# Optimization experiments

Hardware: AMD Instinct MI355X
Metric: run time of the kernel (lower is better)

## Reference

```python
import jax, jax.numpy as jnp
import numpy as np

ORDER = 63
CODEBOOK_SIZE = 256
MIN_DATA = 1
N_ITER = 5
EPS = 1e-05
PERTURB = 1e-05


def setup_inputs() -> dict:
    key = jax.random.key(0)
    x = jax.random.normal(key, (131072, ORDER + 1), dtype=jnp.float32)
    return {"x": x}


def _e_step(x, cb, T):
    # squared euclidean distances via gram trick: (T, curr)
    d2 = jnp.sum(x * x, 1)[:, None] - 2.0 * (x @ cb.T) + jnp.sum(cb * cb, 1)[None, :]
    idx = jnp.argmin(d2, axis=1)
    xq = cb[idx]
    dist = jnp.sum((x - xq) ** 2) / T
    return idx, dist


def _m_step(x, idx, curr, key):
    D = x.shape[1]
    ones = jnp.ones((x.shape[0],), x.dtype)
    n_data = jax.ops.segment_sum(ones, idx, num_segments=curr)        # histc
    mask = n_data >= MIN_DATA
    sums = jax.ops.segment_sum(x, idx, num_segments=curr)             # scatter_add
    cent = sums / jnp.maximum(n_data, 1.0)[:, None]
    m = jnp.argmax(n_data)
    r = jax.random.normal(key, (curr, D), x.dtype) * PERTURB
    nm = (~mask).astype(x.dtype)
    # empty clusters reseeded from the largest cluster, perturbed
    new = jnp.where(mask[:, None], cent, cent[m][None, :] - r)
    cnt = jnp.sum(nm)
    corr = jnp.sum(r * nm[:, None], axis=0) / jnp.maximum(cnt, 1.0)
    new = new.at[m].add(jnp.where(cnt > 0, corr, jnp.zeros_like(corr)))
    return new


def _lbg(x):
    T, D = x.shape
    K = CODEBOOK_SIZE
    codebook = jnp.full((K, D), 1e10, x.dtype).at[0].set(jnp.mean(x, axis=0))
    distance = jnp.asarray(jnp.inf, x.dtype)
    base = jax.random.key(42)
    curr = 1
    split = 0
    while curr * 2 <= K:  # static loop over log2(K) binary splits
        key_s = jax.random.fold_in(base, split)
        kr, kloop = jax.random.split(key_s)
        r = jax.random.normal(kr, (curr, D), x.dtype) * PERTURB
        codebook = codebook.at[curr:2 * curr].set(codebook[:curr] - r).at[:curr].add(r)
        curr *= 2
        prev = distance

        def body(carry, n, curr=curr):
            cb, prev_d, dist, done, key = carry
            idx, d_new = _e_step(x, cb, T)
            change = jnp.abs(prev_d - d_new)
            conv = (n > 0) & (change / (d_new + 1e-16) < EPS)
            key, sub = jax.random.split(key)
            cb_new = _m_step(x, idx, curr, sub)
            stop = done | conv
            cb_out = jnp.where(stop, cb, cb_new)        # skip m-step on convergence/break
            dist_out = jnp.where(done, dist, d_new)     # distance assigned before break
            prev_out = jnp.where(stop, prev_d, d_new)
            return (cb_out, prev_out, dist_out, stop, key), None

        carry0 = (codebook[:curr], prev, distance, jnp.asarray(False), kloop)
        (cb_fin, _, distance, _, _), _ = jax.lax.scan(body, carry0, jnp.arange(N_ITER))
        codebook = codebook.at[:curr].set(cb_fin)
        split += 1
    return codebook, distance


def reference(x):
    return _lbg(x)
```

## Files before the change

### kernel.cpp

```cpp
#include <hip/hip_runtime.h>
#include <stdint.h>


#define NPTS 131072
#define DIMS 64
#define KCB  256
#define NCB  16

struct LbgState { float dist; float prev; unsigned int done; unsigned int k0, k1; unsigned int pad; };

__device__ __forceinline__ uint32_t rotl32(uint32_t v, int n){ return (v<<n)|(v>>(32-n)); }

__device__ __forceinline__ void tf2x32(uint32_t k0, uint32_t k1, uint32_t x0, uint32_t x1,
                                       uint32_t& o0, uint32_t& o1){
  uint32_t ks2 = k0 ^ k1 ^ 0x1BD11BDAu;
  x0 += k0; x1 += k1;
  #define TFR(r) { x0 += x1; x1 = rotl32(x1, r); x1 ^= x0; }
  TFR(13) TFR(15) TFR(26) TFR(6)
  x0 += k1; x1 += ks2 + 1u;
  TFR(17) TFR(29) TFR(16) TFR(24)
  x0 += ks2; x1 += k0 + 2u;
  TFR(13) TFR(15) TFR(26) TFR(6)
  x0 += k0; x1 += k1 + 3u;
  TFR(17) TFR(29) TFR(16) TFR(24)
  x0 += k1; x1 += ks2 + 4u;
  TFR(13) TFR(15) TFR(26) TFR(6)
  x0 += ks2; x1 += k0 + 5u;
  #undef TFR
  o0 = x0; o1 = x1;
}

__device__ __forceinline__ float xla_erfinv_f32(float x){
  float w = -log1pf(-x*x);
  float p;
  if (w < 5.0f){
    w = w - 2.5f;
    p = 2.81022636e-08f;
    p = fmaf(p, w, 3.43273939e-07f);
    p = fmaf(p, w, -3.5233877e-06f);
    p = fmaf(p, w, -4.39150654e-06f);
    p = fmaf(p, w, 0.00021858087f);
    p = fmaf(p, w, -0.00125372503f);
    p = fmaf(p, w, -0.00417768164f);
    p = fmaf(p, w, 0.246640727f);
    p = fmaf(p, w, 1.50140941f);
  } else {
    w = sqrtf(w) - 3.0f;
    p = -0.000200214257f;
    p = fmaf(p, w, 0.000100950558f);
    p = fmaf(p, w, 0.00134934322f);
    p = fmaf(p, w, -0.00367342844f);
    p = fmaf(p, w, 0.00573950773f);
    p = fmaf(p, w, -0.0076224613f);
    p = fmaf(p, w, 0.00943887047f);
    p = fmaf(p, w, 1.00167406f);
    p = fmaf(p, w, 2.83297682f);
  }
  return p * x;
}

__device__ __forceinline__ float jax_normal_elem(uint32_t k0, uint32_t k1, uint32_t j){
  uint32_t o0, o1; tf2x32(k0, k1, 0u, j, o0, o1);
  uint32_t bits = o0 ^ o1;
  uint32_t fb = (bits >> 9) | 0x3f800000u;
  float f = __uint_as_float(fb) - 1.0f;
  const float lo = -0.99999994f;
  float u = f * 2.0f + lo;
  u = fmaxf(lo, u);
  return 1.41421356f * xla_erfinv_f32(u);
}

__device__ void do_split(float* __restrict__ cb, float* __restrict__ cnorm,
                         unsigned long long* __restrict__ sums,
                         unsigned int* __restrict__ ndata,
                         unsigned long long* __restrict__ distacc,
                         LbgState* __restrict__ st, int curr, int split, int t){
  __shared__ uint32_t kr0s, kr1s;
  if (t == 0){
    uint32_t ks0, ks1, a0, a1, b0, b1;
    tf2x32(0u, 42u, 0u, (uint32_t)split, ks0, ks1);
    tf2x32(ks0, ks1, 0u, 0u, a0, a1);
    tf2x32(ks0, ks1, 0u, 1u, b0, b1);
    kr0s = a0; kr1s = a1;
    st->k0 = b0; st->k1 = b1;
    st->prev = st->dist;
    st->done = 0u;
  }
  __syncthreads();
  const int n = curr * DIMS;
  for (int e = t; e < n; e += 256){
    int c = e >> 6, d = e & 63;
    float rv = jax_normal_elem(kr0s, kr1s, (uint32_t)e) * 1e-5f;
    float old = cb[c*DIMS + d];
    cb[(curr + c)*DIMS + d] = old - rv;
    cb[c*DIMS + d]          = old + rv;
  }
  __syncthreads();
  const int c2 = curr * 2;
  for (int c = t; c < c2; c += 256){
    float s = 0.f;
    for (int d = 0; d < DIMS; d++){ float vv = cb[c*DIMS+d]; s += vv*vv; }
    cnorm[c] = s;
  }
  for (int e = t; e < c2*DIMS; e += 256) sums[e] = 0ull;
  for (int c = t; c < c2; c += 256) ndata[c] = 0u;
  if (t == 0) *distacc = 0ull;
}

__global__ void mean_kernel(const float* __restrict__ x, unsigned long long* __restrict__ macc,
                            float* __restrict__ cb, float* __restrict__ cnorm,
                            unsigned long long* __restrict__ sums,
                            unsigned int* __restrict__ ndata,
                            unsigned long long* __restrict__ distacc,
                            LbgState* __restrict__ st, unsigned int* __restrict__ mcnt){
  __shared__ double part[256];
  __shared__ float stage[16*64];
  __shared__ int islast;
  const int t = threadIdx.x;
  const int d = t & 63;
  const int w = t >> 6;
  const size_t base = (size_t)blockIdx.x * 1024;
  const int lrow = t >> 4;
  const int lcol = (t & 15) * 4;

  const float4* xg = reinterpret_cast<const float4*>(x);
  float4 nxt = xg[((base + lrow) * DIMS + lcol) >> 2];
  double s = 0.0;
  for (int tt = 0; tt < 64; tt++){
    float4 cur = nxt;
    if (tt < 63)
      nxt = xg[((base + (tt+1)*16 + lrow) * DIMS + lcol) >> 2];
    __syncthreads();
    *reinterpret_cast<float4*>(&stage[lrow*DIMS + lcol]) = cur;
    __syncthreads();
    s += (double)stage[(w    )*DIMS + d];
    s += (double)stage[(w + 4)*DIMS + d];
    s += (double)stage[(w + 8)*DIMS + d];
    s += (double)stage[(w +12)*DIMS + d];
  }
  part[t] = s;
  __syncthreads();
  if (t < 64){
    double tot = part[t] + part[64+t] + part[128+t] + part[192+t];
    atomicAdd(&macc[t], (unsigned long long)__double2ll_rn(tot * 1099511627776.0));
  }
  __threadfence();
  __syncthreads();
  if (t == 0) islast = (atomicAdd(mcnt, 1u) == (unsigned)(gridDim.x - 1));
  __syncthreads();
  if (!islast) return;

  if (t < 64){
    long long mv = (long long)atomicAdd(&macc[t], 0ull);
    double mean = (double)mv * (1.0/1099511627776.0) / 131072.0;
    cb[t] = (float)mean;
  }
  for (int e = t; e < KCB*DIMS; e += 256)
    if (e >= 64) cb[e] = 1e10f;
  if (t == 0){
    st->dist = __builtin_inff();
    st->prev = __builtin_inff();
    st->done = 0u;
    atomicExch(mcnt, 0u);
  }
  __syncthreads();
  do_split(cb, cnorm, sums, ndata, distacc, st, 1, 0, t);
}

template<int CURR>
__global__ __launch_bounds__(256, 4)
void estep_kernel(const float* __restrict__ x, const float* __restrict__ cb,
                  const float* __restrict__ cnorm, unsigned char* __restrict__ bidx8,
                  unsigned long long* __restrict__ distacc, const LbgState* __restrict__ st){
  if (st->done) return;
  const int t = threadIdx.x;
  const int lane = t & 63;
  const int p = blockIdx.x * 256 + t;

  float xv[DIMS];
  const float4* xp = reinterpret_cast<const float4*>(x + (size_t)p * DIMS);
  #pragma unroll
  for (int i = 0; i < 16; i++){
    float4 v = xp[i];
    xv[4*i+0] = v.x; xv[4*i+1] = v.y; xv[4*i+2] = v.z; xv[4*i+3] = v.w;
  }
  float xx = 0.f;
  #pragma unroll
  for (int d = 0; d < DIMS; d++) xx += xv[d] * xv[d];

  constexpr int NJ = (CURR < 4) ? CURR : 4;
  float best = __builtin_inff();
  int bi = 0;
  for (int j0 = 0; j0 < CURR; j0 += NJ){
    const float* crow = cb + (size_t)j0 * DIMS;
    float acc[NJ];
    #pragma unroll
    for (int k = 0; k < NJ; k++) acc[k] = 0.f;
    #pragma unroll
    for (int d = 0; d < DIMS; d++){
      #pragma unroll
      for (int k = 0; k < NJ; k++)
        acc[k] = fmaf(xv[d], crow[k*DIMS + d], acc[k]);
    }
    #pragma unroll
    for (int k = 0; k < NJ; k++){
      float d2 = (xx - 2.0f*acc[k]) + cnorm[j0 + k];
      if (d2 < best){ best = d2; bi = j0 + k; }
    }
  }
  bidx8[p] = (unsigned char)bi;

  double dd = 0.0;
  const float4* cbv = reinterpret_cast<const float4*>(cb + (size_t)bi * DIMS);
  #pragma unroll
  for (int i = 0; i < 16; i++){
    float4 b = cbv[i];
    float df, sq;
    df = xv[4*i+0] - b.x; sq = df*df; dd += (double)sq;
    df = xv[4*i+1] - b.y; sq = df*df; dd += (double)sq;
    df = xv[4*i+2] - b.z; sq = df*df; dd += (double)sq;
    df = xv[4*i+3] - b.w; sq = df*df; dd += (double)sq;
  }
  for (int off = 32; off > 0; off >>= 1) dd += __shfl_down(dd, off);
  if (lane == 0)
    atomicAdd(distacc, (unsigned long long)__double2ll_rn(dd * 4294967296.0));
}

template<int CURR>
__global__ __launch_bounds__(256, 4)
void estep_sw(const float* __restrict__ x, const float* __restrict__ cb,
              const float* __restrict__ cnorm, unsigned char* __restrict__ bidx8,
              unsigned long long* __restrict__ distacc, const LbgState* __restrict__ st){
  if (st->done) return;
  constexpr int CPW = CURR / 4;
  constexpr int NJG = (CPW < 16) ? CPW : 16;
  constexpr int NG = CPW / NJG;
  __shared__ float4 xs[16*128];
  __shared__ float sxx[128];
  __shared__ float sbest[4*128];
  __shared__ int   sidx [4*128];
  __shared__ unsigned char sbidx[128];
  const int t = threadIdx.x;
  const int lane = t & 63;
  const int w = __builtin_amdgcn_readfirstlane(t >> 6);
  const int pbase = blockIdx.x * 128;

  {
    const int p = t & 127, h = t >> 7;
    const float4* xg = reinterpret_cast<const float4*>(x) + (size_t)(pbase + p) * 16 + h * 8;
    #pragma unroll
    for (int j = 0; j < 8; j++)
      xs[(h*8 + j)*128 + p] = xg[j];
  }
  __syncthreads();
  if (t < 128){
    float xx = 0.f;
    #pragma unroll
    for (int k4 = 0; k4 < 16; k4++){
      float4 v = xs[k4*128 + t];
      xx = fmaf(v.x, v.x, xx); xx = fmaf(v.y, v.y, xx);
      xx = fmaf(v.z, v.z, xx); xx = fmaf(v.w, v.w, xx);
    }
    sxx[t] = xx;
  }
  __syncthreads();

  const float xx0 = sxx[lane];
  const float xx1 = sxx[64 + lane];
  float best0 = __builtin_inff(), best1 = __builtin_inff();
  int bi0 = 0, bi1 = 0;
  const float4* cbg = reinterpret_cast<const float4*>(cb);
  const int cwbase = w * CPW;

  for (int g = 0; g < NG; g++){
    const int c0 = cwbase + g*NJG;
    float acc0[NJG], acc1[NJG];
    #pragma unroll
    for (int cj = 0; cj < NJG; cj++){ acc0[cj] = 0.f; acc1[cj] = 0.f; }
    for (int k4 = 0; k4 < 16; k4++){
      float4 xf0 = xs[k4*128 + lane];
      float4 xf1 = xs[k4*128 + 64 + lane];
      #pragma unroll
      for (int cj = 0; cj < NJG; cj++){
        float4 cf = cbg[(size_t)(c0 + cj)*16 + k4];
        acc0[cj] = fmaf(xf0.x, cf.x, acc0[cj]);
        acc0[cj] = fmaf(xf0.y, cf.y, acc0[cj]);
        acc0[cj] = fmaf(xf0.z, cf.z, acc0[cj]);
        acc0[cj] = fmaf(xf0.w, cf.w, acc0[cj]);
        acc1[cj] = fmaf(xf1.x, cf.x, acc1[cj]);
        acc1[cj] = fmaf(xf1.y, cf.y, acc1[cj]);
        acc1[cj] = fmaf(xf1.z, cf.z, acc1[cj]);
        acc1[cj] = fmaf(xf1.w, cf.w, acc1[cj]);
      }
    }
    #pragma unroll
    for (int cj = 0; cj < NJG; cj++){
      float cn = cnorm[c0 + cj];
      float d20 = (xx0 - 2.0f*acc0[cj]) + cn;
      if (d20 < best0){ best0 = d20; bi0 = c0 + cj; }
      float d21 = (xx1 - 2.0f*acc1[cj]) + cn;
      if (d21 < best1){ best1 = d21; bi1 = c0 + cj; }
    }
  }
  sbest[w*128 + lane]      = best0;  sidx[w*128 + lane]      = bi0;
  sbest[w*128 + 64 + lane] = best1;  sidx[w*128 + 64 + lane] = bi1;
  __syncthreads();

  if (t < 128){
    float best = sbest[t];
    int bi = sidx[t];
    #pragma unroll
    for (int ww = 1; ww < 4; ww++){
      float ob = sbest[ww*128 + t];
      int   oi = sidx [ww*128 + t];
      if (ob < best){ best = ob; bi = oi; }
    }
    sbidx[t] = (unsigned char)bi;
    bidx8[pbase + t] = (unsigned char)bi;
    const float4* cbv = cbg + (size_t)bi * 16;
    double dd = 0.0;
    #pragma unroll
    for (int k4 = 0; k4 < 16; k4++){
      float4 xv = xs[k4*128 + t];
      float4 b = cbv[k4];
      float df, sq;
      df = xv.x - b.x; sq = df*df; dd += (double)sq;
      df = xv.y - b.y; sq = df*df; dd += (double)sq;
      df = xv.z - b.z; sq = df*df; dd += (double)sq;
      df = xv.w - b.w; sq = df*df; dd += (double)sq;
    }
    for (int off = 32; off > 0; off >>= 1) dd += __shfl_down(dd, off);
    if ((t & 63) == 0)
      atomicAdd(distacc, (unsigned long long)__double2ll_rn(dd * 4294967296.0));
  }
}

template<int CURR, int NBLK>
__global__ __launch_bounds__(256)
void gather_kernel(const float* __restrict__ x, const unsigned char* __restrict__ bidx8,
                   unsigned long long* __restrict__ sums, unsigned int* __restrict__ ndata,
                   const LbgState* __restrict__ st){
  if (st->done) return;
  constexpr int CLOG = __builtin_ctz(CURR);
  constexpr int NCHUNK = NBLK / CURR;
  constexpr int PPC = NPTS / NCHUNK;
  constexpr int NPW = PPC / 4;
  __shared__ long long sacc[4][64][4];
  __shared__ unsigned int scw[4];
  const int t = threadIdx.x;
  const int lane = t & 63;
  const int w = t >> 6;
  const int c = blockIdx.x & (CURR - 1);
  const int chunk = blockIdx.x >> CLOG;
  const int pbase = chunk * PPC + w * NPW;
  const int sub = lane >> 4;
  const int dof = (lane & 15) * 4;

  long long a0 = 0, a1 = 0, a2 = 0, a3 = 0;
  unsigned int cnt = 0;
  int q0=0,q1=0,q2=0,q3=0,q4=0,q5=0,q6=0,q7=0, qn=0;
  const uint32_t* bp = reinterpret_cast<const uint32_t*>(bidx8 + pbase);
  for (int i = 0; i < NPW; i += 256){
    const uint32_t b4 = bp[(i >> 2) + lane];
    #pragma unroll
    for (int s = 0; s < 4; s++){
      unsigned long long m = __ballot(((b4 >> (8*s)) & 255u) == (unsigned)c);
      cnt += (unsigned int)__popcll(m);
      while (m){
        const int bit = __builtin_ctzll(m);
        m &= m - 1ull;
        const int p = pbase + i + bit*4 + s;
        if      (qn == 0) q0 = p;
        else if (qn == 1) q1 = p;
        else if (qn == 2) q2 = p;
        else if (qn == 3) q3 = p;
        else if (qn == 4) q4 = p;
        else if (qn == 5) q5 = p;
        else if (qn == 6) q6 = p;
        else              q7 = p;
        qn++;
        if (qn == 8){
          const int rA = (sub==0)?q0:(sub==1)?q1:(sub==2)?q2:q3;
          const int rB = (sub==0)?q4:(sub==1)?q5:(sub==2)?q6:q7;
          const float4 vA = *reinterpret_cast<const float4*>(x + (size_t)rA * DIMS + dof);
          const float4 vB = *reinterpret_cast<const float4*>(x + (size_t)rB * DIMS + dof);
          a0 += (long long)__double2int_rn((double)vA.x * 1048576.0);
          a1 += (long long)__double2int_rn((double)vA.y * 1048576.0);
          a2 += (long long)__double2int_rn((double)vA.z * 1048576.0);
          a3 += (long long)__double2int_rn((double)vA.w * 1048576.0);
          a0 += (long long)__double2int_rn((double)vB.x * 1048576.0);
          a1 += (long long)__double2int_rn((double)vB.y * 1048576.0);
          a2 += (long long)__double2int_rn((double)vB.z * 1048576.0);
          a3 += (long long)__double2int_rn((double)vB.w * 1048576.0);
          qn = 0;
        }
      }
    }
  }
  if (qn > 0){
    const int i1 = (qn > 1) ? q1 : q0;
    const int i2 = (qn > 2) ? q2 : q0;
    const int i3 = (qn > 3) ? q3 : q0;
    const int i4 = (qn > 4) ? q4 : q0;
    const int i5 = (qn > 5) ? q5 : q0;
    const int i6 = (qn > 6) ? q6 : q0;
    const int rA = (sub==0)?q0:(sub==1)?i1:(sub==2)?i2:i3;
    const int rB = (sub==0)?i4:(sub==1)?i5:(sub==2)?i6:q0;
    const float4 vA = *reinterpret_cast<const float4*>(x + (size_t)rA * DIMS + dof);
    const float4 vB = *reinterpret_cast<const float4*>(x + (size_t)rB * DIMS + dof);
    if (sub < qn){
      a0 += (long long)__double2int_rn((double)vA.x * 1048576.0);
      a1 += (long long)__double2int_rn((double)vA.y * 1048576.0);
      a2 += (long long)__double2int_rn((double)vA.z * 1048576.0);
      a3 += (long long)__double2int_rn((double)vA.w * 1048576.0);
    }
    if (sub + 4 < qn){
      a0 += (long long)__double2int_rn((double)vB.x * 1048576.0);
      a1 += (long long)__double2int_rn((double)vB.y * 1048576.0);
      a2 += (long long)__double2int_rn((double)vB.z * 1048576.0);
      a3 += (long long)__double2int_rn((double)vB.w * 1048576.0);
    }
  }
  sacc[w][lane][0] = a0; sacc[w][lane][1] = a1;
  sacc[w][lane][2] = a2; sacc[w][lane][3] = a3;
  if (lane == 0) scw[w] = cnt;
  __syncthreads();
  if (w == 0){
    long long tot = 0;
    #pragma unroll
    for (int ww = 0; ww < 4; ww++)
      #pragma unroll
      for (int r = 0; r < 4; r++)
        tot += sacc[ww][r*16 + (lane >> 2)][lane & 3];
    if (tot) atomicAdd(&sums[c*DIMS + lane], (unsigned long long)(tot * 1048576ll));
    if (lane == 0){
      unsigned int ct = scw[0] + scw[1] + scw[2] + scw[3];
      if (ct) atomicAdd(&ndata[c], ct);
    }
  }
}

__global__ void control_kernel(float* __restrict__ cb, float* __restrict__ cnorm,
                               const unsigned long long* __restrict__ sums_in,
                               unsigned long long* __restrict__ sums_out,
                               const unsigned int* __restrict__ ndata_in,
                               unsigned int* __restrict__ ndata_out,
                               const unsigned long long* __restrict__ distacc_in,
                               unsigned long long* __restrict__ distacc_out,
                               const LbgState* __restrict__ st_in,
                               LbgState* __restrict__ st_out,
                               int curr, int n_iter, int next_split){
  __shared__ float cm[64];
  __shared__ int redv[256];
  __shared__ int redi[256];
  __shared__ int s_m, s_cnt;
  const int t = threadIdx.x;
  const int b = blockIdx.x;

  const unsigned int done0 = st_in->done;
  float d_new = 0.f;
  int stop = 1;
  uint32_t sub0 = 0, sub1 = 0, nk0 = 0, nk1 = 0;
  if (!done0){
    double ddv = (double)(long long)(*distacc_in) * (1.0/4294967296.0);
    float sf = (float)ddv;
    d_new = sf / 131072.0f;
    float change = fabsf(st_in->prev - d_new);
    int conv = (n_iter > 0) && (change / (d_new + 1e-16f) < 1e-5f);
    stop = conv;
    if (!conv){
      tf2x32(st_in->k0, st_in->k1, 0u, 0u, nk0, nk1);
      tf2x32(st_in->k0, st_in->k1, 0u, 1u, sub0, sub1);
    }
  }

  const int rpb = (curr + NCB - 1) / NCB;
  const int r0 = b * rpb;
  int r1 = r0 + rpb; if (r1 > curr) r1 = curr;

  if (!done0 && !stop){
    int v = (t < curr) ? (int)ndata_in[t] : -1;
    redv[t] = v; redi[t] = t;
    __syncthreads();
    for (int s = 128; s > 0; s >>= 1){
      if (t < s){
        if (redv[t+s] > redv[t] || (redv[t+s] == redv[t] && redi[t+s] < redi[t])){
          redv[t] = redv[t+s]; redi[t] = redi[t+s];
        }
      }
      __syncthreads();
    }
    if (t == 0) s_m = redi[0];
    __syncthreads();
    redv[t] = (t < curr && ndata_in[t] == 0u) ? 1 : 0;
    __syncthreads();
    for (int s = 128; s > 0; s >>= 1){
      if (t < s) redv[t] += redv[t+s];
      __syncthreads();
    }
    if (t == 0) s_cnt = redv[0];
    __syncthreads();
    const int m = s_m;
    const int cntE = s_cnt;

    if (t < 64){
      unsigned int nm_ = ndata_in[m]; if (nm_ < 1u) nm_ = 1u;
      double cd = (double)(long long)sums_in[m*DIMS + t] * (1.0/1099511627776.0) / (double)nm_;
      cm[t] = (float)cd;
    }
    __syncthreads();

    for (int e = r0*DIMS + t; e < r1*DIMS; e += 256){
      int cc = e >> 6, d = e & 63;
      if (cc == m) continue;
      float nv;
      unsigned int nd = ndata_in[cc];
      if (nd >= 1u){
        double cd = (double)(long long)sums_in[e] * (1.0/1099511627776.0) / (double)nd;
        nv = (float)cd;
      } else {
        float rv = jax_normal_elem(sub0, sub1, (uint32_t)e) * 1e-5f;
        nv = cm[d] - rv;
      }
      cb[e] = nv;
    }
    if (m >= r0 && m < r1 && t < 64){
      float add = 0.f;
      if (cntE > 0){
        float acc = 0.f;
        for (int cc = 0; cc < curr; cc++){
          if (ndata_in[cc] == 0u)
            acc += jax_normal_elem(sub0, sub1, (uint32_t)(cc*DIMS + t)) * 1e-5f;
        }
        add = acc / fmaxf((float)cntE, 1.0f);
      }
      cb[m*DIMS + t] = cm[t] + add;
    }
    __syncthreads();

    for (int cc = r0 + t; cc < r1; cc += 256){
      float s = 0.f;
      for (int d = 0; d < DIMS; d++){ float vv = cb[cc*DIMS+d]; s += vv*vv; }
      cnorm[cc] = s;
    }
  }

  const int rows_next = (n_iter == 4 && curr < KCB) ? 2*curr : curr;
  for (int e = b*256 + t; e < rows_next*DIMS; e += NCB*256) sums_out[e] = 0ull;
  for (int cc = b*256 + t; cc < rows_next; cc += NCB*256) ndata_out[cc] = 0u;
  if (b == 0 && t == 0) *distacc_out = 0ull;

  if (b == 0 && t == 0){
    const float fin_dist = done0 ? st_in->dist : d_new;
    LbgState ns;
    ns.dist = fin_dist;
    if (done0 || stop){
      ns.prev = st_in->prev; ns.done = 1u; ns.k0 = st_in->k0; ns.k1 = st_in->k1;
    } else {
      ns.prev = d_new; ns.done = 0u; ns.k0 = nk0; ns.k1 = nk1;
    }
    ns.pad = 0u;
    if (n_iter == 4){
      if (curr < KCB){
        uint32_t ks0, ks1, sa0, sa1, sb0, sb1;
        tf2x32(0u, 42u, 0u, (uint32_t)next_split, ks0, ks1);
        tf2x32(ks0, ks1, 0u, 0u, sa0, sa1);
        tf2x32(ks0, ks1, 0u, 1u, sb0, sb1);
        ns.k0 = sb0; ns.k1 = sb1;
        ns.prev = fin_dist;
        ns.done = 0u;
      } else {
        cb[KCB*DIMS] = fin_dist;
      }
    }
    *st_out = ns;
  }

  if (n_iter == 4 && curr < KCB){
    uint32_t ks0, ks1, kr0, kr1, t0, t1;
    tf2x32(0u, 42u, 0u, (uint32_t)next_split, ks0, ks1);
    tf2x32(ks0, ks1, 0u, 0u, kr0, kr1);
    (void)t0; (void)t1;
    __syncthreads();
    for (int e = r0*DIMS + t; e < r1*DIMS; e += 256){
      int cc = e >> 6, d = e & 63;
      float rv = jax_normal_elem(kr0, kr1, (uint32_t)e) * 1e-5f;
      float old = cb[e];
      cb[(curr + cc)*DIMS + d] = old - rv;
      cb[e]                    = old + rv;
    }
    __syncthreads();
    for (int cc = r0 + t; cc < r1; cc += 256){
      float s0 = 0.f, s1 = 0.f;
      for (int d = 0; d < DIMS; d++){
        float v0 = cb[cc*DIMS + d];        s0 += v0*v0;
        float v1 = cb[(curr+cc)*DIMS + d]; s1 += v1*v1;
      }
      cnorm[cc] = s0;
      cnorm[curr + cc] = s1;
    }
  }
}

extern "C" void kernel_launch(void* const* d_in, const int* in_sizes, int n_in,
                              void* d_out, int out_size, void* d_ws, size_t ws_size,
                              hipStream_t stream){
  const float* x = (const float*)d_in[0];
  float* cb = (float*)d_out;
  char* ws = (char*)d_ws;
  unsigned long long* sums0   = (unsigned long long*)(ws + 0);
  unsigned long long* sums1   = (unsigned long long*)(ws + 131072);
  unsigned long long* macc    = (unsigned long long*)(ws + 262144);
  unsigned long long* dist0   = (unsigned long long*)(ws + 262656);
  unsigned long long* dist1   = (unsigned long long*)(ws + 262664);
  LbgState* st0               = (LbgState*)(ws + 262672);
  LbgState* st1               = (LbgState*)(ws + 262704);
  unsigned int* nd0           = (unsigned int*)(ws + 262736);
  unsigned int* nd1           = (unsigned int*)(ws + 263760);
  float* cnorm                = (float*)(ws + 264784);
  unsigned char* bidx8        = (unsigned char*)(ws + 265808);
  unsigned int* mcnt          = (unsigned int*)(ws + 396880);

  unsigned long long* sums[2] = { sums0, sums1 };
  unsigned long long* dac[2]  = { dist0, dist1 };
  LbgState* st[2]             = { st0, st1 };
  unsigned int* nd[2]         = { nd0, nd1 };

  hipMemsetAsync(d_ws, 0, 396884, stream);
  mean_kernel<<<128, 256, 0, stream>>>(x, macc, cb, cnorm, sums0, nd0, dist0, st0, mcnt);

  int g = 0;
  for (int split = 0; split < 8; split++){
    const int curr = 2 << split;
    for (int n = 0; n < 5; n++){
      const int pi = g & 1, po = pi ^ 1;
      switch (curr){
        case 2:   estep_kernel<2>  <<<512,256,0,stream>>>(x,cb,cnorm,bidx8,dac[pi],st[pi]);
                  gather_kernel<2,256>   <<<256, 256,0,stream>>>(x,bidx8,sums[pi],nd[pi],st[pi]); break;
        case 4:   estep_kernel<4>  <<<512,256,0,stream>>>(x,cb,cnorm,bidx8,dac[pi],st[pi]);
                  gather_kernel<4,512>   <<<512, 256,0,stream>>>(x,bidx8,sums[pi],nd[pi],st[pi]); break;
        case 8:   estep_sw<8>    <<<1024,256,0,stream>>>(x,cb,cnorm,bidx8,dac[pi],st[pi]);
                  gather_kernel<8,1024>  <<<1024,256,0,stream>>>(x,bidx8,sums[pi],nd[pi],st[pi]); break;
        case 16:  estep_sw<16>   <<<1024,256,0,stream>>>(x,cb,cnorm,bidx8,dac[pi],st[pi]);
                  gather_kernel<16,2048> <<<2048,256,0,stream>>>(x,bidx8,sums[pi],nd[pi],st[pi]); break;
        case 32:  estep_sw<32>   <<<1024,256,0,stream>>>(x,cb,cnorm,bidx8,dac[pi],st[pi]);
                  gather_kernel<32,2048> <<<2048,256,0,stream>>>(x,bidx8,sums[pi],nd[pi],st[pi]); break;
        case 64:  estep_sw<64>   <<<1024,256,0,stream>>>(x,cb,cnorm,bidx8,dac[pi],st[pi]);
                  gather_kernel<64,2048> <<<2048,256,0,stream>>>(x,bidx8,sums[pi],nd[pi],st[pi]); break;
        case 128: estep_sw<128>  <<<1024,256,0,stream>>>(x,cb,cnorm,bidx8,dac[pi],st[pi]);
                  gather_kernel<128,2048><<<2048,256,0,stream>>>(x,bidx8,sums[pi],nd[pi],st[pi]); break;
        case 256: estep_sw<256>  <<<1024,256,0,stream>>>(x,cb,cnorm,bidx8,dac[pi],st[pi]);
                  gather_kernel<256,2048><<<2048,256,0,stream>>>(x,bidx8,sums[pi],nd[pi],st[pi]); break;
      }
      control_kernel<<<NCB, 256, 0, stream>>>(cb, cnorm,
          sums[pi], sums[po], nd[pi], nd[po], dac[pi], dac[po],
          st[pi], st[po], curr, n, split+1);
      g++;
    }
  }
}
```

Baseline: 2.721 ms.

## Fuse control step into gather kernel via last-block-done pattern

Merges the separate control kernel into the gather kernel. A global atomic counter picks the last finishing block, which then runs the centroid update, reseeding and codebook norms alone. Zeroing of the next iteration's accumulators is spread across all gather blocks. This removes one kernel launch and its launch gap per iteration (40 total), but the control work now runs serially in a single block instead of 16, and it adds a threadfence plus volatile loads.

```diff
diff --git a/kernel.cpp b/kernel.cpp
--- a/kernel.cpp
+++ b/kernel.cpp
@@ -5,11 +5,17 @@
 #define NPTS 131072
 #define DIMS 64
 #define KCB  256
-#define NCB  16
 
 struct LbgState { float dist; float prev; unsigned int done; unsigned int k0, k1; unsigned int pad; };
 
 __device__ __forceinline__ uint32_t rotl32(uint32_t v, int n){ return (v<<n)|(v>>(32-n)); }
+
+__device__ __forceinline__ unsigned long long vload64(const unsigned long long* p){
+  return *(volatile const unsigned long long*)p;
+}
+__device__ __forceinline__ unsigned int vload32(const unsigned int* p){
+  return *(volatile const unsigned int*)p;
+}
 
 __device__ __forceinline__ void tf2x32(uint32_t k0, uint32_t k1, uint32_t x0, uint32_t x1,
                                        uint32_t& o0, uint32_t& o1){
@@ -335,134 +341,24 @@
   }
 }
 
-template<int CURR, int NBLK>
-__global__ __launch_bounds__(256)
-void gather_kernel(const float* __restrict__ x, const unsigned char* __restrict__ bidx8,
-                   unsigned long long* __restrict__ sums, unsigned int* __restrict__ ndata,
-                   const LbgState* __restrict__ st){
-  if (st->done) return;
-  constexpr int CLOG = __builtin_ctz(CURR);
-  constexpr int NCHUNK = NBLK / CURR;
-  constexpr int PPC = NPTS / NCHUNK;
-  constexpr int NPW = PPC / 4;
-  __shared__ long long sacc[4][64][4];
-  __shared__ unsigned int scw[4];
-  const int t = threadIdx.x;
-  const int lane = t & 63;
-  const int w = t >> 6;
-  const int c = blockIdx.x & (CURR - 1);
-  const int chunk = blockIdx.x >> CLOG;
-  const int pbase = chunk * PPC + w * NPW;
-  const int sub = lane >> 4;
-  const int dof = (lane & 15) * 4;
-
-  long long a0 = 0, a1 = 0, a2 = 0, a3 = 0;
-  unsigned int cnt = 0;
-  int q0=0,q1=0,q2=0,q3=0,q4=0,q5=0,q6=0,q7=0, qn=0;
-  const uint32_t* bp = reinterpret_cast<const uint32_t*>(bidx8 + pbase);
-  for (int i = 0; i < NPW; i += 256){
-    const uint32_t b4 = bp[(i >> 2) + lane];
-    #pragma unroll
-    for (int s = 0; s < 4; s++){
-      unsigned long long m = __ballot(((b4 >> (8*s)) & 255u) == (unsigned)c);
-      cnt += (unsigned int)__popcll(m);
-      while (m){
-        const int bit = __builtin_ctzll(m);
-        m &= m - 1ull;
-        const int p = pbase + i + bit*4 + s;
-        if      (qn == 0) q0 = p;
-        else if (qn == 1) q1 = p;
-        else if (qn == 2) q2 = p;
-        else if (qn == 3) q3 = p;
-        else if (qn == 4) q4 = p;
-        else if (qn == 5) q5 = p;
-        else if (qn == 6) q6 = p;
-        else              q7 = p;
-        qn++;
-        if (qn == 8){
-          const int rA = (sub==0)?q0:(sub==1)?q1:(sub==2)?q2:q3;
-          const int rB = (sub==0)?q4:(sub==1)?q5:(sub==2)?q6:q7;
-          const float4 vA = *reinterpret_cast<const float4*>(x + (size_t)rA * DIMS + dof);
-          const float4 vB = *reinterpret_cast<const float4*>(x + (size_t)rB * DIMS + dof);
-          a0 += (long long)__double2int_rn((double)vA.x * 1048576.0);
-          a1 += (long long)__double2int_rn((double)vA.y * 1048576.0);
-          a2 += (long long)__double2int_rn((double)vA.z * 1048576.0);
-          a3 += (long long)__double2int_rn((double)vA.w * 1048576.0);
-          a0 += (long long)__double2int_rn((double)vB.x * 1048576.0);
-          a1 += (long long)__double2int_rn((double)vB.y * 1048576.0);
-          a2 += (long long)__double2int_rn((double)vB.z * 1048576.0);
-          a3 += (long long)__double2int_rn((double)vB.w * 1048576.0);
-          qn = 0;
-        }
-      }
-    }
-  }
-  if (qn > 0){
-    const int i1 = (qn > 1) ? q1 : q0;
-    const int i2 = (qn > 2) ? q2 : q0;
-    const int i3 = (qn > 3) ? q3 : q0;
-    const int i4 = (qn > 4) ? q4 : q0;
-    const int i5 = (qn > 5) ? q5 : q0;
-    const int i6 = (qn > 6) ? q6 : q0;
-    const int rA = (sub==0)?q0:(sub==1)?i1:(sub==2)?i2:i3;
-    const int rB = (sub==0)?i4:(sub==1)?i5:(sub==2)?i6:q0;
-    const float4 vA = *reinterpret_cast<const float4*>(x + (size_t)rA * DIMS + dof);
-    const float4 vB = *reinterpret_cast<const float4*>(x + (size_t)rB * DIMS + dof);
-    if (sub < qn){
-      a0 += (long long)__double2int_rn((double)vA.x * 1048576.0);
-      a1 += (long long)__double2int_rn((double)vA.y * 1048576.0);
-      a2 += (long long)__double2int_rn((double)vA.z * 1048576.0);
-      a3 += (long long)__double2int_rn((double)vA.w * 1048576.0);
-    }
-    if (sub + 4 < qn){
-      a0 += (long long)__double2int_rn((double)vB.x * 1048576.0);
-      a1 += (long long)__double2int_rn((double)vB.y * 1048576.0);
-      a2 += (long long)__double2int_rn((double)vB.z * 1048576.0);
-      a3 += (long long)__double2int_rn((double)vB.w * 1048576.0);
-    }
-  }
-  sacc[w][lane][0] = a0; sacc[w][lane][1] = a1;
-  sacc[w][lane][2] = a2; sacc[w][lane][3] = a3;
-  if (lane == 0) scw[w] = cnt;
-  __syncthreads();
-  if (w == 0){
-    long long tot = 0;
-    #pragma unroll
-    for (int ww = 0; ww < 4; ww++)
-      #pragma unroll
-      for (int r = 0; r < 4; r++)
-        tot += sacc[ww][r*16 + (lane >> 2)][lane & 3];
-    if (tot) atomicAdd(&sums[c*DIMS + lane], (unsigned long long)(tot * 1048576ll));
-    if (lane == 0){
-      unsigned int ct = scw[0] + scw[1] + scw[2] + scw[3];
-      if (ct) atomicAdd(&ndata[c], ct);
-    }
-  }
-}
-
-__global__ void control_kernel(float* __restrict__ cb, float* __restrict__ cnorm,
-                               const unsigned long long* __restrict__ sums_in,
-                               unsigned long long* __restrict__ sums_out,
-                               const unsigned int* __restrict__ ndata_in,
-                               unsigned int* __restrict__ ndata_out,
-                               const unsigned long long* __restrict__ distacc_in,
-                               unsigned long long* __restrict__ distacc_out,
-                               const LbgState* __restrict__ st_in,
-                               LbgState* __restrict__ st_out,
-                               int curr, int n_iter, int next_split){
+__device__ void control_tail(float* __restrict__ cb, float* __restrict__ cnorm,
+                             const unsigned long long* __restrict__ sums_in,
+                             const unsigned int* __restrict__ ndata_in,
+                             const unsigned long long* __restrict__ distacc_in,
+                             const LbgState* __restrict__ st_in,
+                             LbgState* __restrict__ st_out,
+                             int curr, int n_iter, int next_split, int t){
   __shared__ float cm[64];
   __shared__ int redv[256];
   __shared__ int redi[256];
   __shared__ int s_m, s_cnt;
-  const int t = threadIdx.x;
-  const int b = blockIdx.x;
 
   const unsigned int done0 = st_in->done;
   float d_new = 0.f;
   int stop = 1;
   uint32_t sub0 = 0, sub1 = 0, nk0 = 0, nk1 = 0;
   if (!done0){
-    double ddv = (double)(long long)(*distacc_in) * (1.0/4294967296.0);
+    double ddv = (double)(long long)vload64(distacc_in) * (1.0/4294967296.0);
     float sf = (float)ddv;
     d_new = sf / 131072.0f;
     float change = fabsf(st_in->prev - d_new);
@@ -474,12 +370,8 @@
     }
   }
 
-  const int rpb = (curr + NCB - 1) / NCB;
-  const int r0 = b * rpb;
-  int r1 = r0 + rpb; if (r1 > curr) r1 = curr;
-
   if (!done0 && !stop){
-    int v = (t < curr) ? (int)ndata_in[t] : -1;
+    int v = (t < curr) ? (int)vload32(&ndata_in[t]) : -1;
     redv[t] = v; redi[t] = t;
     __syncthreads();
     for (int s = 128; s > 0; s >>= 1){
@@ -492,7 +384,7 @@
     }
     if (t == 0) s_m = redi[0];
     __syncthreads();
-    redv[t] = (t < curr && ndata_in[t] == 0u) ? 1 : 0;
+    redv[t] = (t < curr && vload32(&ndata_in[t]) == 0u) ? 1 : 0;
     __syncthreads();
     for (int s = 128; s > 0; s >>= 1){
       if (t < s) redv[t] += redv[t+s];
@@ -504,19 +396,20 @@
     const int cntE = s_cnt;
 
     if (t < 64){
-      unsigned int nm_ = ndata_in[m]; if (nm_ < 1u) nm_ = 1u;
-      double cd = (double)(long long)sums_in[m*DIMS + t] * (1.0/1099511627776.0) / (double)nm_;
+      unsigned int nm_ = vload32(&ndata_in[m]); if (nm_ < 1u) nm_ = 1u;
+      double cd = (double)(long long)vload64(&sums_in[m*DIMS + t]) * (1.0/1099511627776.0) / (double)nm_;
       cm[t] = (float)cd;
     }
     __syncthreads();
 
-    for (int e = r0*DIMS + t; e < r1*DIMS; e += 256){
+    const int total = curr * DIMS;
+    for (int e = t; e < total; e += 256){
       int cc = e >> 6, d = e & 63;
       if (cc == m) continue;
       float nv;
-      unsigned int nd = ndata_in[cc];
+      unsigned int nd = vload32(&ndata_in[cc]);
       if (nd >= 1u){
-        double cd = (double)(long long)sums_in[e] * (1.0/1099511627776.0) / (double)nd;
+        double cd = (double)(long long)vload64(&sums_in[e]) * (1.0/1099511627776.0) / (double)nd;
         nv = (float)cd;
       } else {
         float rv = jax_normal_elem(sub0, sub1, (uint32_t)e) * 1e-5f;
@@ -524,12 +417,12 @@
       }
       cb[e] = nv;
     }
-    if (m >= r0 && m < r1 && t < 64){
+    if (t < 64){
       float add = 0.f;
       if (cntE > 0){
         float acc = 0.f;
         for (int cc = 0; cc < curr; cc++){
-          if (ndata_in[cc] == 0u)
+          if (vload32(&ndata_in[cc]) == 0u)
             acc += jax_normal_elem(sub0, sub1, (uint32_t)(cc*DIMS + t)) * 1e-5f;
         }
         add = acc / fmaxf((float)cntE, 1.0f);
@@ -538,19 +431,14 @@
     }
     __syncthreads();
 
-    for (int cc = r0 + t; cc < r1; cc += 256){
+    for (int cc = t; cc < curr; cc += 256){
       float s = 0.f;
       for (int d = 0; d < DIMS; d++){ float vv = cb[cc*DIMS+d]; s += vv*vv; }
       cnorm[cc] = s;
     }
   }
 
-  const int rows_next = (n_iter == 4 && curr < KCB) ? 2*curr : curr;
-  for (int e = b*256 + t; e < rows_next*DIMS; e += NCB*256) sums_out[e] = 0ull;
-  for (int cc = b*256 + t; cc < rows_next; cc += NCB*256) ndata_out[cc] = 0u;
-  if (b == 0 && t == 0) *distacc_out = 0ull;
-
-  if (b == 0 && t == 0){
+  if (t == 0){
     const float fin_dist = done0 ? st_in->dist : d_new;
     LbgState ns;
     ns.dist = fin_dist;
@@ -577,12 +465,11 @@
   }
 
   if (n_iter == 4 && curr < KCB){
-    uint32_t ks0, ks1, kr0, kr1, t0, t1;
+    uint32_t ks0, ks1, kr0, kr1;
     tf2x32(0u, 42u, 0u, (uint32_t)next_split, ks0, ks1);
     tf2x32(ks0, ks1, 0u, 0u, kr0, kr1);
-    (void)t0; (void)t1;
-    __syncthreads();
-    for (int e = r0*DIMS + t; e < r1*DIMS; e += 256){
+    __syncthreads();
+    for (int e = t; e < curr*DIMS; e += 256){
       int cc = e >> 6, d = e & 63;
       float rv = jax_normal_elem(kr0, kr1, (uint32_t)e) * 1e-5f;
       float old = cb[e];
@@ -590,7 +477,7 @@
       cb[e]                    = old + rv;
     }
     __syncthreads();
-    for (int cc = r0 + t; cc < r1; cc += 256){
+    for (int cc = t; cc < curr; cc += 256){
       float s0 = 0.f, s1 = 0.f;
       for (int d = 0; d < DIMS; d++){
         float v0 = cb[cc*DIMS + d];        s0 += v0*v0;
@@ -600,6 +487,139 @@
       cnorm[curr + cc] = s1;
     }
   }
+}
+
+template<int CURR, int NBLK>
+__global__ __launch_bounds__(256)
+void gatherc_kernel(const float* __restrict__ x, const unsigned char* __restrict__ bidx8,
+                    unsigned long long* __restrict__ sums, unsigned int* __restrict__ ndata,
+                    unsigned long long* __restrict__ sums_out, unsigned int* __restrict__ ndata_out,
+                    unsigned long long* __restrict__ distacc, unsigned long long* __restrict__ distacc_out,
+                    const LbgState* __restrict__ st, LbgState* __restrict__ st_out,
+                    float* __restrict__ cb, float* __restrict__ cnorm,
+                    int n_iter, int next_split, unsigned int* __restrict__ gcnt){
+  constexpr int CLOG = __builtin_ctz(CURR);
+  constexpr int NCHUNK = NBLK / CURR;
+  constexpr int PPC = NPTS / NCHUNK;
+  constexpr int NPW = PPC / 4;
+  __shared__ long long sacc[4][64][4];
+  __shared__ unsigned int scw[4];
+  __shared__ int islast;
+  const int t = threadIdx.x;
+  const int lane = t & 63;
+  const int w = t >> 6;
+  const unsigned int done = st->done;
+
+  {
+    const int rows_next = (n_iter == 4 && CURR < KCB) ? 2*CURR : CURR;
+    for (int e = blockIdx.x*256 + t; e < rows_next*DIMS; e += NBLK*256) sums_out[e] = 0ull;
+    for (int cc = blockIdx.x*256 + t; cc < rows_next; cc += NBLK*256) ndata_out[cc] = 0u;
+    if (blockIdx.x == 0 && t == 0) *distacc_out = 0ull;
+  }
+
+  if (!done){
+    const int c = blockIdx.x & (CURR - 1);
+    const int chunk = blockIdx.x >> CLOG;
+    const int pbase = chunk * PPC + w * NPW;
+    const int sub = lane >> 4;
+    const int dof = (lane & 15) * 4;
+
+    long long a0 = 0, a1 = 0, a2 = 0, a3 = 0;
+    unsigned int cnt = 0;
+    int q0=0,q1=0,q2=0,q3=0,q4=0,q5=0,q6=0,q7=0, qn=0;
+    const uint32_t* bp = reinterpret_cast<const uint32_t*>(bidx8 + pbase);
+    for (int i = 0; i < NPW; i += 256){
+      const uint32_t b4 = bp[(i >> 2) + lane];
+      #pragma unroll
+      for (int s = 0; s < 4; s++){
+        unsigned long long m = __ballot(((b4 >> (8*s)) & 255u) == (unsigned)c);
+        cnt += (unsigned int)__popcll(m);
+        while (m){
+          const int bit = __builtin_ctzll(m);
+          m &= m - 1ull;
+          const int p = pbase + i + bit*4 + s;
+          if      (qn == 0) q0 = p;
+          else if (qn == 1) q1 = p;
+          else if (qn == 2) q2 = p;
+          else if (qn == 3) q3 = p;
+          else if (qn == 4) q4 = p;
+          else if (qn == 5) q5 = p;
+          else if (qn == 6) q6 = p;
+          else              q7 = p;
+          qn++;
+          if (qn == 8){
+            const int rA = (sub==0)?q0:(sub==1)?q1:(sub==2)?q2:q3;
+            const int rB = (sub==0)?q4:(sub==1)?q5:(sub==2)?q6:q7;
+            const float4 vA = *reinterpret_cast<const float4*>(x + (size_t)rA * DIMS + dof);
+            const float4 vB = *reinterpret_cast<const float4*>(x + (size_t)rB * DIMS + dof);
+            a0 += (long long)__double2int_rn((double)vA.x * 1048576.0);
+            a1 += (long long)__double2int_rn((double)vA.y * 1048576.0);
+            a2 += (long long)__double2int_rn((double)vA.z * 1048576.0);
+            a3 += (long long)__double2int_rn((double)vA.w * 1048576.0);
+            a0 += (long long)__double2int_rn((double)vB.x * 1048576.0);
+            a1 += (long long)__double2int_rn((double)vB.y * 1048576.0);
+            a2 += (long long)__double2int_rn((double)vB.z * 1048576.0);
+            a3 += (long long)__double2int_rn((double)vB.w * 1048576.0);
+            qn = 0;
+          }
+        }
+      }
+    }
+    if (qn > 0){
+      const int i1 = (qn > 1) ? q1 : q0;
+      const int i2 = (qn > 2) ? q2 : q0;
+      const int i3 = (qn > 3) ? q3 : q0;
+      const int i4 = (qn > 4) ? q4 : q0;
+      const int i5 = (qn > 5) ? q5 : q0;
+      const int i6 = (qn > 6) ? q6 : q0;
+      const int rA = (sub==0)?q0:(sub==1)?i1:(sub==2)?i2:i3;
+      const int rB = (sub==0)?i4:(sub==1)?i5:(sub==2)?i6:q0;
+      const float4 vA = *reinterpret_cast<const float4*>(x + (size_t)rA * DIMS + dof);
+      const float4 vB = *reinterpret_cast<const float4*>(x + (size_t)rB * DIMS + dof);
+      if (sub < qn){
+        a0 += (long long)__double2int_rn((double)vA.x * 1048576.0);
+        a1 += (long long)__double2int_rn((double)vA.y * 1048576.0);
+        a2 += (long long)__double2int_rn((double)vA.z * 1048576.0);
+        a3 += (long long)__double2int_rn((double)vA.w * 1048576.0);
+      }
+      if (sub + 4 < qn){
+        a0 += (long long)__double2int_rn((double)vB.x * 1048576.0);
+        a1 += (long long)__double2int_rn((double)vB.y * 1048576.0);
+        a2 += (long long)__double2int_rn((double)vB.z * 1048576.0);
+        a3 += (long long)__double2int_rn((double)vB.w * 1048576.0);
+      }
+    }
+    sacc[w][lane][0] = a0; sacc[w][lane][1] = a1;
+    sacc[w][lane][2] = a2; sacc[w][lane][3] = a3;
+    if (lane == 0) scw[w] = cnt;
+    __syncthreads();
+    if (w == 0){
+      long long tot = 0;
+      #pragma unroll
+      for (int ww = 0; ww < 4; ww++)
+        #pragma unroll
+        for (int r = 0; r < 4; r++)
+          tot += sacc[ww][r*16 + (lane >> 2)][lane & 3];
+      if (tot) atomicAdd(&sums[c*DIMS + lane], (unsigned long long)(tot * 1048576ll));
+      if (lane == 0){
+        unsigned int ct = scw[0] + scw[1] + scw[2] + scw[3];
+        if (ct) atomicAdd(&ndata[c], ct);
+      }
+    }
+  }
+
+  __threadfence();
+  __syncthreads();
+  if (t == 0){
+    unsigned int old = atomicAdd(gcnt, 1u);
+    islast = (old == (unsigned)(NBLK - 1));
+    if (islast) atomicExch(gcnt, 0u);
+  }
+  __syncthreads();
+  if (!islast) return;
+
+  control_tail(cb, cnorm, sums, ndata, distacc, st, st_out,
+               CURR, n_iter, next_split, t);
 }
 
 extern "C" void kernel_launch(void* const* d_in, const int* in_sizes, int n_in,
@@ -620,13 +640,14 @@
   float* cnorm                = (float*)(ws + 264784);
   unsigned char* bidx8        = (unsigned char*)(ws + 265808);
   unsigned int* mcnt          = (unsigned int*)(ws + 396880);
+  unsigned int* gcnt          = (unsigned int*)(ws + 396884);
 
   unsigned long long* sums[2] = { sums0, sums1 };
   unsigned long long* dac[2]  = { dist0, dist1 };
   LbgState* st[2]             = { st0, st1 };
   unsigned int* nd[2]         = { nd0, nd1 };
 
-  hipMemsetAsync(d_ws, 0, 396884, stream);
+  hipMemsetAsync(d_ws, 0, 396888, stream);
   mean_kernel<<<128, 256, 0, stream>>>(x, macc, cb, cnorm, sums0, nd0, dist0, st0, mcnt);
 
   int g = 0;
@@ -635,26 +656,39 @@
     for (int n = 0; n < 5; n++){
       const int pi = g & 1, po = pi ^ 1;
       switch (curr){
-        case 2:   estep_kernel<2>  <<<512,256,0,stream>>>(x,cb,cnorm,bidx8,dac[pi],st[pi]);
-                  gather_kernel<2,256>   <<<256, 256,0,stream>>>(x,bidx8,sums[pi],nd[pi],st[pi]); break;
-        case 4:   estep_kernel<4>  <<<512,256,0,stream>>>(x,cb,cnorm,bidx8,dac[pi],st[pi]);
-                  gather_kernel<4,512>   <<<512, 256,0,stream>>>(x,bidx8,sums[pi],nd[pi],st[pi]); break;
-        case 8:   estep_sw<8>    <<<1024,256,0,stream>>>(x,cb,cnorm,bidx8,dac[pi],st[pi]);
-                  gather_kernel<8,1024>  <<<1024,256,0,stream>>>(x,bidx8,sums[pi],nd[pi],st[pi]); break;
-        case 16:  estep_sw<16>   <<<1024,256,0,stream>>>(x,cb,cnorm,bidx8,dac[pi],st[pi]);
-                  gather_kernel<16,2048> <<<2048,256,0,stream>>>(x,bidx8,sums[pi],nd[pi],st[pi]); break;
-        case 32:  estep_sw<32>   <<<1024,256,0,stream>>>(x,cb,cnorm,bidx8,dac[pi],st[pi]);
-                  gather_kernel<32,2048> <<<2048,256,0,stream>>>(x,bidx8,sums[pi],nd[pi],st[pi]); break;
-        case 64:  estep_sw<64>   <<<1024,256,0,stream>>>(x,cb,cnorm,bidx8,dac[pi],st[pi]);
-                  gather_kernel<64,2048> <<<2048,256,0,stream>>>(x,bidx8,sums[pi],nd[pi],st[pi]); break;
-        case 128: estep_sw<128>  <<<1024,256,0,stream>>>(x,cb,cnorm,bidx8,dac[pi],st[pi]);
-                  gather_kernel<128,2048><<<2048,256,0,stream>>>(x,bidx8,sums[pi],nd[pi],st[pi]); break;
-        case 256: estep_sw<256>  <<<1024,256,0,stream>>>(x,cb,cnorm,bidx8,dac[pi],st[pi]);
-                  gather_kernel<256,2048><<<2048,256,0,stream>>>(x,bidx8,sums[pi],nd[pi],st[pi]); break;
-      }
-      control_kernel<<<NCB, 256, 0, stream>>>(cb, cnorm,
-          sums[pi], sums[po], nd[pi], nd[po], dac[pi], dac[po],
-          st[pi], st[po], curr, n, split+1);
+        case 2:
+          estep_kernel<2><<<512,256,0,stream>>>(x,cb,cnorm,bidx8,dac[pi],st[pi]);
+          gatherc_kernel<2,256><<<256,256,0,stream>>>(x,bidx8,sums[pi],nd[pi],sums[po],nd[po],
+              dac[pi],dac[po],st[pi],st[po],cb,cnorm,n,split+1,gcnt); break;
+        case 4:
+          estep_kernel<4><<<512,256,0,stream>>>(x,cb,cnorm,bidx8,dac[pi],st[pi]);
+          gatherc_kernel<4,512><<<512,256,0,stream>>>(x,bidx8,sums[pi],nd[pi],sums[po],nd[po],
+              dac[pi],dac[po],st[pi],st[po],cb,cnorm,n,split+1,gcnt); break;
+        case 8:
+          estep_sw<8><<<1024,256,0,stream>>>(x,cb,cnorm,bidx8,dac[pi],st[pi]);
+          gatherc_kernel<8,1024><<<1024,256,0,stream>>>(x,bidx8,sums[pi],nd[pi],sums[po],nd[po],
+              dac[pi],dac[po],st[pi],st[po],cb,cnorm,n,split+1,gcnt); break;
+        case 16:
+          estep_sw<16><<<1024,256,0,stream>>>(x,cb,cnorm,bidx8,dac[pi],st[pi]);
+          gatherc_kernel<16,2048><<<2048,256,0,stream>>>(x,bidx8,sums[pi],nd[pi],sums[po],nd[po],
+              dac[pi],dac[po],st[pi],st[po],cb,cnorm,n,split+1,gcnt); break;
+        case 32:
+          estep_sw<32><<<1024,256,0,stream>>>(x,cb,cnorm,bidx8,dac[pi],st[pi]);
+          gatherc_kernel<32,2048><<<2048,256,0,stream>>>(x,bidx8,sums[pi],nd[pi],sums[po],nd[po],
+              dac[pi],dac[po],st[pi],st[po],cb,cnorm,n,split+1,gcnt); break;
+        case 64:
+          estep_sw<64><<<1024,256,0,stream>>>(x,cb,cnorm,bidx8,dac[pi],st[pi]);
+          gatherc_kernel<64,2048><<<2048,256,0,stream>>>(x,bidx8,sums[pi],nd[pi],sums[po],nd[po],
+              dac[pi],dac[po],st[pi],st[po],cb,cnorm,n,split+1,gcnt); break;
+        case 128:
+          estep_sw<128><<<1024,256,0,stream>>>(x,cb,cnorm,bidx8,dac[pi],st[pi]);
+          gatherc_kernel<128,2048><<<2048,256,0,stream>>>(x,bidx8,sums[pi],nd[pi],sums[po],nd[po],
+              dac[pi],dac[po],st[pi],st[po],cb,cnorm,n,split+1,gcnt); break;
+        case 256:
+          estep_sw<256><<<1024,256,0,stream>>>(x,cb,cnorm,bidx8,dac[pi],st[pi]);
+          gatherc_kernel<256,2048><<<2048,256,0,stream>>>(x,bidx8,sums[pi],nd[pi],sums[po],nd[po],
+              dac[pi],dac[po],st[pi],st[po],cb,cnorm,n,split+1,gcnt); break;
+      }
       g++;
     }
   }
```

New measurement: 7.013 ms. +157.7%, slower.
